# Performance work log

Hardware: AMD Instinct MI355X
Metric: run time of the kernel (lower is better)

## Reference

```python
import jax, jax.numpy as jnp
import numpy as np

EMB = 256
HID = 1024
N_TRACKS = 4096
SEQ = 9
SCALE = 4.0


def setup_inputs() -> dict:
    key = jax.random.key(0)
    ks = jax.random.split(key, 12)

    def init(k, shape, fan_in):
        b = 1.0 / np.sqrt(fan_in)
        return jax.random.uniform(k, shape, jnp.float32, -b, b)

    return {
        "observed": jax.random.normal(ks[0], (SEQ, N_TRACKS, 2), jnp.float32),
        "emb_w": init(ks[1], (EMB - 2, 2), 2),
        "emb_b": init(ks[2], (EMB - 2,), 2),
        "enc_wih": init(ks[3], (4 * HID, EMB), HID),
        "enc_whh": init(ks[4], (4 * HID, HID), HID),
        "enc_b": init(ks[5], (4 * HID,), HID),
        "dec_wih": init(ks[6], (4 * HID, EMB), HID),
        "dec_whh": init(ks[7], (4 * HID, HID), HID),
        "dec_b": init(ks[8], (4 * HID,), HID),
        "h2n_w": init(ks[9], (5, HID), HID),
        "h2n_b": init(ks[10], (5,), HID),
        "n_predict": 12,
    }


def _forward(observed, emb_w, emb_b, enc_wih, enc_whh, enc_b,
             dec_wih, dec_whh, dec_b, h2n_w, h2n_b, n_predict):
    n = observed.shape[1]
    H = enc_whh.shape[1]
    E = enc_wih.shape[1]

    def cell(x, h, c, wih, whh, b):
        # PyTorch LSTMCell gate order: i, f, g, o
        g = x @ wih.T + h @ whh.T + b
        i, f, gg, o = jnp.split(g, 4, axis=-1)
        c = jax.nn.sigmoid(f) * c + jax.nn.sigmoid(i) * jnp.tanh(gg)
        h = jax.nn.sigmoid(o) * jnp.tanh(c)
        return h, c

    def embed(v):
        # Linear(2, E-2) -> ReLU, then 2 zero tag channels
        e = jax.nn.relu((v * SCALE) @ emb_w.T + emb_b)
        return jnp.concatenate([e, jnp.zeros((v.shape[0], 2), e.dtype)], axis=1)

    def h2n(h):
        raw = h @ h2n_w.T + h2n_b
        sig = 0.01 + 0.2 * jax.nn.sigmoid(raw[:, 2:4])  # sigma1, sigma2
        rho = 0.7 * jax.nn.sigmoid(raw[:, 4:5])          # rho
        return jnp.concatenate([raw[:, :2], sig, rho], axis=1)

    def step(params, h, c, obs1, obs2):
        wih, whh, b = params
        mask = ~(jnp.isnan(obs1[:, 0]) | jnp.isnan(obs2[:, 0]))  # [N]
        x = embed(obs2 - obs1)
        h2, c2 = cell(x, h, c, wih, whh, b)
        nrm = h2n(h2)
        m = mask[:, None]
        h = jnp.where(m, h2, h)
        c = jnp.where(m, c2, c)
        normal = jnp.where(m, nrm, jnp.nan)
        pos = obs2 + normal[:, :2]
        return h, c, normal, pos

    h = jnp.zeros((n, H), observed.dtype)
    c = jnp.zeros((n, H), observed.dtype)

    # encoder start tag
    tag_enc = jnp.zeros((n, E), observed.dtype).at[:, -2].set(1.0)
    h, c = cell(tag_enc, h, c, enc_wih, enc_whh, enc_b)

    enc_p = (enc_wih, enc_whh, enc_b)

    def enc_scan(carry, obs_pair):
        h, c = carry
        o1, o2 = obs_pair
        h, c, normal, pos = step(enc_p, h, c, o1, o2)
        return (h, c), (normal, pos)

    (h, c), (enc_normals, enc_positions) = jax.lax.scan(
        enc_scan, (h, c), (observed[:-1], observed[1:]))

    # decoder start tag
    tag_dec = jnp.zeros((n, E), observed.dtype).at[:, -1].set(1.0)
    h, c = cell(tag_dec, h, c, dec_wih, dec_whh, dec_b)

    dec_p = (dec_wih, dec_whh, dec_b)
    p1, p2 = enc_positions[-2], enc_positions[-1]

    def dec_scan(carry, _):
        h, c, p1, p2 = carry
        o1 = jax.lax.stop_gradient(p1)  # .detach() in torch
        o2 = jax.lax.stop_gradient(p2)
        h, c, normal, pos = step(dec_p, h, c, o1, o2)
        return (h, c, p2, pos), (normal, pos)

    _, (dec_normals, dec_positions) = jax.lax.scan(
        dec_scan, (h, c, p1, p2), None, length=n_predict - 1)

    rel_pred_scene = jnp.concatenate([enc_normals, dec_normals], axis=0)
    pred_scene = jnp.concatenate([enc_positions, dec_positions], axis=0)
    return rel_pred_scene, pred_scene


def reference(observed, emb_w, emb_b, enc_wih, enc_whh, enc_b,
              dec_wih, dec_whh, dec_b, h2n_w, h2n_b, n_predict):
    return _forward(observed, emb_w, emb_b, enc_wih, enc_whh, enc_b,
                    dec_wih, dec_whh, dec_b, h2n_w, h2n_b, n_predict)
```

## Files before the change

### kernel.cpp

```cpp
#include <hip/hip_runtime.h>
#include <stdint.h>

#define NTRK 4096
#define HIDN 1024
#define EMBN 256
#define KTOT 1280
#define NOUT 19

typedef __attribute__((ext_vector_type(8))) short short8;
typedef __attribute__((ext_vector_type(4))) float f32x4;

typedef __attribute__((address_space(1))) const void GV;
typedef __attribute__((address_space(3))) void LV;

__device__ __forceinline__ uint16_t f2bf(float f) {
  uint32_t u = __float_as_uint(f);
  u += 0x7fffu + ((u >> 16) & 1u);
  return (uint16_t)(u >> 16);
}
__device__ __forceinline__ float bf2f(uint16_t v) {
  return __uint_as_float(((uint32_t)v) << 16);
}
__device__ __forceinline__ float sigm(float x) { return 1.0f / (1.0f + expf(-x)); }
__device__ __forceinline__ float sigmf_(float x) {
  return __builtin_amdgcn_rcpf(1.0f + __expf(-x));
}
__device__ __forceinline__ float tanhf_(float x) {
  return 2.0f * __builtin_amdgcn_rcpf(1.0f + __expf(-2.0f * x)) - 1.0f;
}

__global__ __launch_bounds__(256) void prep_weights(
    const float* __restrict__ encWih, const float* __restrict__ encWhh,
    const float* __restrict__ encB,
    const float* __restrict__ decWih, const float* __restrict__ decWhh,
    const float* __restrict__ decB,
    uint16_t* __restrict__ WihpE, uint16_t* __restrict__ WhhpE,
    uint16_t* __restrict__ WihpD, uint16_t* __restrict__ WhhpD,
    float* __restrict__ biasE, float* __restrict__ biasD, float* __restrict__ biasDT)
{
  const int jp = blockIdx.x;
  const int q = jp >> 6, r = jp & 63;
  const int gate = r >> 4, l16 = r & 15;
  const int u = q * 16 + l16;
  const int orig = gate * 1024 + u;
  const int t = threadIdx.x;

  WihpE[(size_t)jp * 256 + t] = f2bf(encWih[(size_t)orig * 256 + t]);
  WihpD[(size_t)jp * 256 + t] = f2bf(decWih[(size_t)orig * 256 + t]);
#pragma unroll
  for (int c = 0; c < 4; c++) {
    WhhpE[(size_t)jp * 1024 + c * 256 + t] = f2bf(encWhh[(size_t)orig * 1024 + c * 256 + t]);
    WhhpD[(size_t)jp * 1024 + c * 256 + t] = f2bf(decWhh[(size_t)orig * 1024 + c * 256 + t]);
  }
  if (t == 0) {
    biasE[jp]  = encB[orig];
    biasD[jp]  = decB[orig];
    biasDT[jp] = decB[orig] + decWih[(size_t)orig * 256 + 255];
  }
}

__global__ void init_h0(const float* __restrict__ encWih, const float* __restrict__ encB,
                        float* __restrict__ h0, float* __restrict__ c0)
{
  const int u = blockIdx.x * 256 + threadIdx.x;
  if (u >= 1024) return;
  const float gi = encWih[(size_t)(u) * 256 + 254]        + encB[u];
  const float gg = encWih[(size_t)(2048 + u) * 256 + 254] + encB[2048 + u];
  const float go = encWih[(size_t)(3072 + u) * 256 + 254] + encB[3072 + u];
  const float c = sigm(gi) * tanhf(gg);
  c0[u] = c;
  h0[u] = sigm(go) * tanhf(c);
}

__global__ void fill_state(const float* __restrict__ h0, const float* __restrict__ c0,
                           uint16_t* __restrict__ H, float* __restrict__ Cst)
{
  const size_t i = (size_t)blockIdx.x * 256 + threadIdx.x;
  const int u = (int)(i & 1023);
  H[i] = f2bf(h0[u]);
  Cst[i] = c0[u];
}

__global__ __launch_bounds__(256) void embed_k(
    const float* __restrict__ o1, const float* __restrict__ o2,
    const float* __restrict__ ew, const float* __restrict__ eb,
    uint16_t* __restrict__ X)
{
  const int trk = blockIdx.x;
  const int j = threadIdx.x;
  const float vx = (o2[trk * 2]     - o1[trk * 2])     * 4.0f;
  const float vy = (o2[trk * 2 + 1] - o1[trk * 2 + 1]) * 4.0f;
  float e = 0.f;
  if (j < 254) e = fmaxf(vx * ew[j * 2] + vy * ew[j * 2 + 1] + eb[j], 0.f);
  X[(size_t)trk * 256 + j] = f2bf(e);
}

__global__ __launch_bounds__(256) void embed8(
    const float* __restrict__ observed, const float* __restrict__ ew,
    const float* __restrict__ eb, uint16_t* __restrict__ Xall)
{
  const int t = blockIdx.y;
  const int trk = blockIdx.x;
  const int j = threadIdx.x;
  const float* o1 = observed + ((size_t)t * 4096 + trk) * 2;
  const float* o2 = o1 + 4096 * 2;
  const float vx = (o2[0] - o1[0]) * 4.0f;
  const float vy = (o2[1] - o1[1]) * 4.0f;
  float e = 0.f;
  if (j < 254) e = fmaxf(vx * ew[j * 2] + vy * ew[j * 2 + 1] + eb[j], 0.f);
  Xall[((size_t)t * 4096 + trk) * 256 + j] = f2bf(e);
}

__global__ __launch_bounds__(256) void gemm_lstm(
    const uint16_t* __restrict__ X,   const uint16_t* __restrict__ Hin,
    const uint16_t* __restrict__ Wih, const uint16_t* __restrict__ Whh,
    const float* __restrict__ bias,   float* __restrict__ Cst,
    uint16_t* __restrict__ Hout,
    const float* __restrict__ obs1,   const float* __restrict__ obs2,
    int k0, int maskmode)
{
  __shared__ uint16_t As[128 * 64];
  __shared__ uint16_t Bs[128 * 64];
  __shared__ uint8_t  smask[128];

  const int tid  = threadIdx.x;
  const int wave = tid >> 6;
  const int lane = tid & 63;
  const int bm = blockIdx.y * 128;
  const int bn = blockIdx.x * 128;

  if (tid < 128) {
    bool m = true;
    if (maskmode) {
      const int row = bm + tid;
      const float a = obs1[row * 2];
      const float b = obs2[row * 2];
      m = !((a != a) || (b != b));
    }
    smask[tid] = m ? 1 : 0;
  }

  const int wrow = wave >> 1;
  const int wcol = wave & 1;
  const int quad = lane >> 4;
  const int l15  = lane & 15;
  const int m7   = l15 & 7;
  const int lr = lane >> 3;
  const int lj = ((lane & 7) ^ lr) * 8;

  f32x4 acc[4][4];
#pragma unroll
  for (int i = 0; i < 4; i++)
#pragma unroll
    for (int j = 0; j < 4; j++) acc[i][j] = (f32x4){0.f, 0.f, 0.f, 0.f};

  auto mfma_slab = [&]() {
#pragma unroll
    for (int kk = 0; kk < 64; kk += 32) {
      short8 af[4], bf[4];
      const int jc = (((kk >> 3) + quad) ^ m7) * 8;
#pragma unroll
      for (int i = 0; i < 4; i++) {
        af[i] = *(const short8*)(As + (wrow * 64 + i * 16 + l15) * 64 + jc);
        bf[i] = *(const short8*)(Bs + (wcol * 64 + i * 16 + l15) * 64 + jc);
      }
#pragma unroll
      for (int i = 0; i < 4; i++)
#pragma unroll
        for (int j = 0; j < 4; j++)
          acc[i][j] = __builtin_amdgcn_mfma_f32_16x16x32_bf16(af[i], bf[j], acc[i][j], 0, 0, 0);
    }
  };

  if (k0 == 0) {
    for (int kt = 0; kt < 256; kt += 64) {
      __syncthreads();
#pragma unroll
      for (int cc = 0; cc < 8; cc++) {
        const bool isA = cc < 4;
        const int trow = ((cc & 3) * 4 + wave) * 8;
        const int grow = (isA ? bm : bn) + trow + lr;
        const uint16_t* gsrc = (isA ? X : Wih) + (size_t)grow * 256 + (kt + lj);
        uint16_t* lbase = (isA ? As : Bs) + trow * 64;
        __builtin_amdgcn_global_load_lds((GV*)gsrc, (LV*)lbase, 16, 0, 0);
      }
      __syncthreads();
      mfma_slab();
    }
  }

  for (int kt = 0; kt < 1024; kt += 64) {
    __syncthreads();
#pragma unroll
    for (int cc = 0; cc < 8; cc++) {
      const bool isA = cc < 4;
      const int trow = ((cc & 3) * 4 + wave) * 8;
      const int grow = (isA ? bm : bn) + trow + lr;
      const uint16_t* gsrc = (isA ? Hin : Whh) + (size_t)grow * 1024 + (kt + lj);
      uint16_t* lbase = (isA ? As : Bs) + trow * 64;
      __builtin_amdgcn_global_load_lds((GV*)gsrc, (LV*)lbase, 16, 0, 0);
    }
    __syncthreads();
    mfma_slab();
  }

  const int u  = ((bn >> 6) + wcol) * 16 + l15;
  const int jb = bn + wcol * 64 + l15;
  const float b_i = bias[jb];
  const float b_f = bias[jb + 16];
  const float b_g = bias[jb + 32];
  const float b_o = bias[jb + 48];

#pragma unroll
  for (int mi = 0; mi < 4; mi++) {
#pragma unroll
    for (int r = 0; r < 4; r++) {
      const int row = bm + wrow * 64 + mi * 16 + quad * 4 + r;
      const size_t idx = (size_t)row * 1024 + u;
      uint16_t hv;
      if (smask[row - bm]) {
        const float gi = acc[mi][0][r] + b_i;
        const float gf = acc[mi][1][r] + b_f;
        const float gg = acc[mi][2][r] + b_g;
        const float go = acc[mi][3][r] + b_o;
        const float cn = sigmf_(gf) * Cst[idx] + sigmf_(gi) * tanhf_(gg);
        Cst[idx] = cn;
        hv = f2bf(sigmf_(go) * tanhf_(cn));
      } else {
        hv = Hin[idx];
      }
      Hout[idx] = hv;
    }
  }
}

__global__ __launch_bounds__(256) void h2n_pos(
    const uint16_t* __restrict__ H, const float* __restrict__ w5, const float* __restrict__ b5,
    const float* __restrict__ obs1, const float* __restrict__ obs2,
    float* __restrict__ outrel, float* __restrict__ outpos,
    const float* __restrict__ pprev, const float* __restrict__ ew,
    const float* __restrict__ eb, uint16_t* __restrict__ Xnext, int do_embed)
{
  const int lane  = threadIdx.x & 63;
  const int track = blockIdx.x * 4 + (threadIdx.x >> 6);

  const uint16_t* hrow = H + (size_t)track * 1024 + lane * 16;
  const short8 v0 = *(const short8*)(hrow);
  const short8 v1 = *(const short8*)(hrow + 8);
  float hv[16];
#pragma unroll
  for (int j = 0; j < 8; j++) {
    hv[j]     = bf2f((uint16_t)v0[j]);
    hv[8 + j] = bf2f((uint16_t)v1[j]);
  }
  const int kb = lane * 16;
  float p[5];
#pragma unroll
  for (int o = 0; o < 5; o++) {
    const float* wr = w5 + (size_t)o * 1024 + kb;
    float s = 0.f;
#pragma unroll
    for (int j = 0; j < 16; j++) s += hv[j] * wr[j];
    p[o] = s;
  }
#pragma unroll
  for (int o = 0; o < 5; o++) {
    float v = p[o];
    v += __shfl_xor(v, 32); v += __shfl_xor(v, 16); v += __shfl_xor(v, 8);
    v += __shfl_xor(v, 4);  v += __shfl_xor(v, 2);  v += __shfl_xor(v, 1);
    p[o] = v;
  }
  const float o1x = obs1[track * 2];
  const float o2x = obs2[track * 2];
  const float o2y = obs2[track * 2 + 1];
  const bool msk = !((o1x != o1x) || (o2x != o2x));
  float n0 = p[0] + b5[0];
  float n1 = p[1] + b5[1];
  float n2 = 0.01f + 0.2f * sigmf_(p[2] + b5[2]);
  float n3 = 0.01f + 0.2f * sigmf_(p[3] + b5[3]);
  float n4 = 0.7f  * sigmf_(p[4] + b5[4]);
  if (!msk) {
    const float qn = __uint_as_float(0x7fc00000u);
    n0 = n1 = n2 = n3 = n4 = qn;
  }
  const float posx = o2x + n0;
  const float posy = o2y + n1;
  if (lane == 0) {
    float* rr = outrel + (size_t)track * 5;
    rr[0] = n0; rr[1] = n1; rr[2] = n2; rr[3] = n3; rr[4] = n4;
    outpos[track * 2]     = posx;
    outpos[track * 2 + 1] = posy;
  }
  if (do_embed) {
    const float vx = (posx - pprev[track * 2])     * 4.0f;
    const float vy = (posy - pprev[track * 2 + 1]) * 4.0f;
    uint16_t* xr = Xnext + (size_t)track * 256;
#pragma unroll
    for (int ii = 0; ii < 4; ii++) {
      const int j = ii * 64 + lane;
      float e = 0.f;
      if (j < 254) e = fmaxf(vx * ew[j * 2] + vy * ew[j * 2 + 1] + eb[j], 0.f);
      xr[j] = f2bf(e);
    }
  }
}

extern "C" void kernel_launch(void* const* d_in, const int* in_sizes, int n_in,
                              void* d_out, int out_size, void* d_ws, size_t ws_size,
                              hipStream_t stream)
{
  const float* observed = (const float*)d_in[0];
  const float* emb_w    = (const float*)d_in[1];
  const float* emb_b    = (const float*)d_in[2];
  const float* enc_wih  = (const float*)d_in[3];
  const float* enc_whh  = (const float*)d_in[4];
  const float* enc_b    = (const float*)d_in[5];
  const float* dec_wih  = (const float*)d_in[6];
  const float* dec_whh  = (const float*)d_in[7];
  const float* dec_b    = (const float*)d_in[8];
  const float* h2n_w    = (const float*)d_in[9];
  const float* h2n_b    = (const float*)d_in[10];

  char* ws = (char*)d_ws;
  size_t off = 0;
  auto alloc = [&](size_t bytes) -> void* {
    size_t cur = (off + 255) & ~(size_t)255;
    off = cur + bytes;
    return (void*)(ws + cur);
  };
  uint16_t* WihpE = (uint16_t*)alloc((size_t)4096 * 256 * 2);
  uint16_t* WhhpE = (uint16_t*)alloc((size_t)4096 * 1024 * 2);
  uint16_t* WihpD = (uint16_t*)alloc((size_t)4096 * 256 * 2);
  uint16_t* WhhpD = (uint16_t*)alloc((size_t)4096 * 1024 * 2);
  float*    biasE = (float*)alloc(4096 * 4);
  float*    biasD = (float*)alloc(4096 * 4);
  float*    biasDT= (float*)alloc(4096 * 4);
  float*    h0    = (float*)alloc(1024 * 4);
  float*    c0    = (float*)alloc(1024 * 4);
  uint16_t* HA    = (uint16_t*)alloc((size_t)4096 * 1024 * 2);
  uint16_t* HB    = (uint16_t*)alloc((size_t)4096 * 1024 * 2);
  float*    Cst   = (float*)alloc((size_t)4096 * 1024 * 4);
  uint16_t* Xb    = (uint16_t*)alloc((size_t)4096 * 256 * 2);
  const size_t xall_bytes = (size_t)8 * 4096 * 256 * 2;
  const bool use_xall = (off + 256 + xall_bytes) <= ws_size;
  uint16_t* Xall = use_xall ? (uint16_t*)alloc(xall_bytes) : nullptr;

  float* outrel = (float*)d_out;
  float* outpos = outrel + (size_t)NOUT * 4096 * 5;

  prep_weights<<<4096, 256, 0, stream>>>(enc_wih, enc_whh, enc_b, dec_wih, dec_whh, dec_b,
                                         WihpE, WhhpE, WihpD, WhhpD, biasE, biasD, biasDT);
  init_h0<<<4, 256, 0, stream>>>(enc_wih, enc_b, h0, c0);
  fill_state<<<16384, 256, 0, stream>>>(h0, c0, HA, Cst);
  if (use_xall) {
    embed8<<<dim3(4096, 8), 256, 0, stream>>>(observed, emb_w, emb_b, Xall);
  }

  uint16_t* Hin = HA;
  uint16_t* Hout = HB;
  const dim3 ggrid(32, 32);

  for (int t = 0; t < 8; t++) {
    const float* o1 = observed + (size_t)t * 4096 * 2;
    const float* o2 = observed + (size_t)(t + 1) * 4096 * 2;
    uint16_t* Xt = Xb;
    if (use_xall) {
      Xt = Xall + (size_t)t * 4096 * 256;
    } else {
      embed_k<<<4096, 256, 0, stream>>>(o1, o2, emb_w, emb_b, Xb);
    }
    gemm_lstm<<<ggrid, 256, 0, stream>>>(Xt, Hin, WihpE, WhhpE, biasE, Cst, Hout, o1, o2, 0, 1);
    const int de = (t == 7) ? 1 : 0;
    h2n_pos<<<1024, 256, 0, stream>>>(Hout, h2n_w, h2n_b, o1, o2,
                                      outrel + (size_t)t * 4096 * 5,
                                      outpos + (size_t)t * 4096 * 2,
                                      outpos + (size_t)6 * 4096 * 2, emb_w, emb_b, Xb, de);
    uint16_t* tmp = Hin; Hin = Hout; Hout = tmp;
  }

  gemm_lstm<<<ggrid, 256, 0, stream>>>(nullptr, Hin, WihpD, WhhpD, biasDT, Cst, Hout,
                                       nullptr, nullptr, 256, 0);
  { uint16_t* tmp = Hin; Hin = Hout; Hout = tmp; }

  for (int s = 0; s < 11; s++) {
    const float* p1 = outpos + (size_t)(6 + s) * 4096 * 2;
    const float* p2 = outpos + (size_t)(7 + s) * 4096 * 2;
    gemm_lstm<<<ggrid, 256, 0, stream>>>(Xb, Hin, WihpD, WhhpD, biasD, Cst, Hout, p1, p2, 0, 1);
    const int de = (s < 10) ? 1 : 0;
    h2n_pos<<<1024, 256, 0, stream>>>(Hout, h2n_w, h2n_b, p1, p2,
                                      outrel + (size_t)(8 + s) * 4096 * 5,
                                      outpos + (size_t)(8 + s) * 4096 * 2,
                                      p2, emb_w, emb_b, Xb, de);
    uint16_t* tmp = Hin; Hin = Hout; Hout = tmp;
  }
}
```

Before: 1.460 ms.

## Rewrite LSTM GEMM with 256x256 tiles, 4-stage LDS pipeline and concatenated weights

The input and recurrent weights are packed into one concatenated bf16 matrix of width 1280, so a single K loop covers both parts. The LSTM GEMM kernel moves from 128x128 tiles with 256 threads to 256x256 tiles with 512 threads. It adds a 4-buffer asynchronous global-to-LDS pipeline with three tiles prefetched, plus a remapped block order for better L2 locality. Dummy loads keep the vmcnt bookkeeping uniform at the tail. The goal is to hide load latency and raise operand reuse, at the cost of 128 KB+ of LDS, heavy register pressure from 32 accumulators per lane, and a grid of only 256 blocks.

```diff
diff --git a/kernel.cpp b/kernel.cpp
--- a/kernel.cpp
+++ b/kernel.cpp
@@ -34,8 +34,7 @@
     const float* __restrict__ encB,
     const float* __restrict__ decWih, const float* __restrict__ decWhh,
     const float* __restrict__ decB,
-    uint16_t* __restrict__ WihpE, uint16_t* __restrict__ WhhpE,
-    uint16_t* __restrict__ WihpD, uint16_t* __restrict__ WhhpD,
+    uint16_t* __restrict__ WcatE, uint16_t* __restrict__ WcatD,
     float* __restrict__ biasE, float* __restrict__ biasD, float* __restrict__ biasDT)
 {
   const int jp = blockIdx.x;
@@ -45,12 +44,12 @@
   const int orig = gate * 1024 + u;
   const int t = threadIdx.x;
 
-  WihpE[(size_t)jp * 256 + t] = f2bf(encWih[(size_t)orig * 256 + t]);
-  WihpD[(size_t)jp * 256 + t] = f2bf(decWih[(size_t)orig * 256 + t]);
+  WcatE[(size_t)jp * KTOT + t] = f2bf(encWih[(size_t)orig * 256 + t]);
+  WcatD[(size_t)jp * KTOT + t] = f2bf(decWih[(size_t)orig * 256 + t]);
 #pragma unroll
   for (int c = 0; c < 4; c++) {
-    WhhpE[(size_t)jp * 1024 + c * 256 + t] = f2bf(encWhh[(size_t)orig * 1024 + c * 256 + t]);
-    WhhpD[(size_t)jp * 1024 + c * 256 + t] = f2bf(decWhh[(size_t)orig * 1024 + c * 256 + t]);
+    WcatE[(size_t)jp * KTOT + 256 + c * 256 + t] = f2bf(encWhh[(size_t)orig * 1024 + c * 256 + t]);
+    WcatD[(size_t)jp * KTOT + 256 + c * 256 + t] = f2bf(decWhh[(size_t)orig * 1024 + c * 256 + t]);
   }
   if (t == 0) {
     biasE[jp]  = encB[orig];
@@ -111,111 +110,123 @@
   Xall[((size_t)t * 4096 + trk) * 256 + j] = f2bf(e);
 }
 
-__global__ __launch_bounds__(256) void gemm_lstm(
-    const uint16_t* __restrict__ X,   const uint16_t* __restrict__ Hin,
-    const uint16_t* __restrict__ Wih, const uint16_t* __restrict__ Whh,
-    const float* __restrict__ bias,   float* __restrict__ Cst,
-    uint16_t* __restrict__ Hout,
-    const float* __restrict__ obs1,   const float* __restrict__ obs2,
+__global__ __launch_bounds__(512, 2) void gemm_lstm(
+    const uint16_t* __restrict__ X,    const uint16_t* __restrict__ Hin,
+    const uint16_t* __restrict__ Wcat, const float* __restrict__ bias,
+    float* __restrict__ Cst,           uint16_t* __restrict__ Hout,
+    const float* __restrict__ obs1,    const float* __restrict__ obs2,
     int k0, int maskmode)
 {
-  __shared__ uint16_t As[128 * 64];
-  __shared__ uint16_t Bs[128 * 64];
-  __shared__ uint8_t  smask[128];
+  __shared__ uint16_t As[4 * 8192];
+  __shared__ uint16_t Bs[4 * 8192];
+  __shared__ uint16_t Dm[4096];
+  __shared__ uint8_t  smask[256];
 
   const int tid  = threadIdx.x;
-  const int wave = tid >> 6;
+  const int w    = tid >> 6;
   const int lane = tid & 63;
-  const int bm = blockIdx.y * 128;
-  const int bn = blockIdx.x * 128;
-
-  if (tid < 128) {
+  const int wr   = w >> 2;
+  const int wc   = w & 3;
+  const int quad = lane >> 4;
+  const int l15  = lane & 15;
+
+  const int bid = blockIdx.y * 16 + blockIdx.x;
+  const int wg  = (bid & 7) * 32 + (bid >> 3);
+  const int bm  = (wg >> 4) * 256;
+  const int bn  = (wg & 15) * 256;
+
+  const int NT = (KTOT - k0) >> 5;
+
+  if (tid < 256) {
     bool m = true;
     if (maskmode) {
-      const int row = bm + tid;
-      const float a = obs1[row * 2];
-      const float b = obs2[row * 2];
+      const float a = obs1[(bm + tid) * 2];
+      const float b = obs2[(bm + tid) * 2];
       m = !((a != a) || (b != b));
     }
     smask[tid] = m ? 1 : 0;
   }
 
-  const int wrow = wave >> 1;
-  const int wcol = wave & 1;
-  const int quad = lane >> 4;
-  const int l15  = lane & 15;
-  const int m7   = l15 & 7;
-  const int lr = lane >> 3;
-  const int lj = ((lane & 7) ^ lr) * 8;
-
-  f32x4 acc[4][4];
-#pragma unroll
-  for (int i = 0; i < 4; i++)
+  const int srow = w * 16 + (lane >> 2);
+  const int kch  = (lane & 3) * 8;
+  const uint16_t* pXa = X ? (X + (size_t)(bm + srow) * 256 + kch) : (const uint16_t*)0;
+  const uint16_t* pHa = Hin  + (size_t)(bm + srow) * 1024 + kch;
+  const uint16_t* pBa = Wcat + (size_t)(bn + srow) * (size_t)KTOT + kch;
+  const int ldsw = w * 16 * 32;
+
+  auto stage_tile = [&](int V) {
+    if (V >= NT) {
+      const GV* dsrc = (GV*)(Wcat + (size_t)tid * 8);
+      LV* ddst = (LV*)(Dm + w * 512);
+#pragma unroll
+      for (int uu = 0; uu < 4; uu++)
+        __builtin_amdgcn_global_load_lds(dsrc, ddst, 16, 0, 0);
+      return;
+    }
+    const int kg = k0 + V * 32;
+    uint16_t* asl = As + (V & 3) * 8192;
+    uint16_t* bsl = Bs + (V & 3) * 8192;
+    const uint16_t* a0;
+    int rstride;
+    if (kg < 256) { a0 = pXa + kg;         rstride = 256;  }
+    else          { a0 = pHa + (kg - 256); rstride = 1024; }
+    __builtin_amdgcn_global_load_lds((GV*)a0,                        (LV*)(asl + ldsw),        16, 0, 0);
+    __builtin_amdgcn_global_load_lds((GV*)(a0 + 128 * rstride),      (LV*)(asl + 4096 + ldsw), 16, 0, 0);
+    const uint16_t* b0 = pBa + kg;
+    __builtin_amdgcn_global_load_lds((GV*)b0,                        (LV*)(bsl + ldsw),        16, 0, 0);
+    __builtin_amdgcn_global_load_lds((GV*)(b0 + 128 * KTOT),         (LV*)(bsl + 4096 + ldsw), 16, 0, 0);
+  };
+
+  f32x4 acc[8][4];
+#pragma unroll
+  for (int i = 0; i < 8; i++)
 #pragma unroll
     for (int j = 0; j < 4; j++) acc[i][j] = (f32x4){0.f, 0.f, 0.f, 0.f};
 
-  auto mfma_slab = [&]() {
-#pragma unroll
-    for (int kk = 0; kk < 64; kk += 32) {
-      short8 af[4], bf[4];
-      const int jc = (((kk >> 3) + quad) ^ m7) * 8;
-#pragma unroll
-      for (int i = 0; i < 4; i++) {
-        af[i] = *(const short8*)(As + (wrow * 64 + i * 16 + l15) * 64 + jc);
-        bf[i] = *(const short8*)(Bs + (wcol * 64 + i * 16 + l15) * 64 + jc);
-      }
-#pragma unroll
-      for (int i = 0; i < 4; i++)
-#pragma unroll
-        for (int j = 0; j < 4; j++)
-          acc[i][j] = __builtin_amdgcn_mfma_f32_16x16x32_bf16(af[i], bf[j], acc[i][j], 0, 0, 0);
-    }
-  };
-
-  if (k0 == 0) {
-    for (int kt = 0; kt < 256; kt += 64) {
-      __syncthreads();
-#pragma unroll
-      for (int cc = 0; cc < 8; cc++) {
-        const bool isA = cc < 4;
-        const int trow = ((cc & 3) * 4 + wave) * 8;
-        const int grow = (isA ? bm : bn) + trow + lr;
-        const uint16_t* gsrc = (isA ? X : Wih) + (size_t)grow * 256 + (kt + lj);
-        uint16_t* lbase = (isA ? As : Bs) + trow * 64;
-        __builtin_amdgcn_global_load_lds((GV*)gsrc, (LV*)lbase, 16, 0, 0);
-      }
-      __syncthreads();
-      mfma_slab();
-    }
-  }
-
-  for (int kt = 0; kt < 1024; kt += 64) {
-    __syncthreads();
-#pragma unroll
-    for (int cc = 0; cc < 8; cc++) {
-      const bool isA = cc < 4;
-      const int trow = ((cc & 3) * 4 + wave) * 8;
-      const int grow = (isA ? bm : bn) + trow + lr;
-      const uint16_t* gsrc = (isA ? Hin : Whh) + (size_t)grow * 1024 + (kt + lj);
-      uint16_t* lbase = (isA ? As : Bs) + trow * 64;
-      __builtin_amdgcn_global_load_lds((GV*)gsrc, (LV*)lbase, 16, 0, 0);
-    }
-    __syncthreads();
-    mfma_slab();
-  }
-
-  const int u  = ((bn >> 6) + wcol) * 16 + l15;
-  const int jb = bn + wcol * 64 + l15;
+  stage_tile(0); stage_tile(1); stage_tile(2);
+  asm volatile("s_waitcnt vmcnt(8)" ::: "memory");
+  __builtin_amdgcn_s_barrier();
+
+  const int aoff = (wr * 128 + l15) * 32 + quad * 8;
+  const int boff = (wc * 64  + l15) * 32 + quad * 8;
+
+  for (int T = 0; T < NT; ++T) {
+    stage_tile(T + 3);
+    const uint16_t* asl = As + (T & 3) * 8192;
+    const uint16_t* bsl = Bs + (T & 3) * 8192;
+    short8 bf[4], af[8];
+#pragma unroll
+    for (int n = 0; n < 4; n++)
+      bf[n] = *(const short8*)(bsl + boff + n * 512);
+#pragma unroll
+    for (int m = 0; m < 8; m++)
+      af[m] = *(const short8*)(asl + aoff + m * 512);
+    __builtin_amdgcn_s_setprio(1);
+#pragma unroll
+    for (int m = 0; m < 8; m++)
+#pragma unroll
+      for (int n = 0; n < 4; n++)
+        acc[m][n] = __builtin_amdgcn_mfma_f32_16x16x32_bf16(af[m], bf[n], acc[m][n], 0, 0, 0);
+    __builtin_amdgcn_s_setprio(0);
+    asm volatile("s_waitcnt lgkmcnt(0)" ::: "memory");
+    __builtin_amdgcn_sched_barrier(0);
+    asm volatile("s_waitcnt vmcnt(8)" ::: "memory");
+    __builtin_amdgcn_s_barrier();
+  }
+  asm volatile("s_waitcnt vmcnt(0)" ::: "memory");
+
+  const int u  = ((bn >> 6) + wc) * 16 + l15;
+  const int jb = bn + wc * 64 + l15;
   const float b_i = bias[jb];
   const float b_f = bias[jb + 16];
   const float b_g = bias[jb + 32];
   const float b_o = bias[jb + 48];
 
 #pragma unroll
-  for (int mi = 0; mi < 4; mi++) {
+  for (int mi = 0; mi < 8; mi++) {
 #pragma unroll
     for (int r = 0; r < 4; r++) {
-      const int row = bm + wrow * 64 + mi * 16 + quad * 4 + r;
+      const int row = bm + wr * 128 + mi * 16 + quad * 4 + r;
       const size_t idx = (size_t)row * 1024 + u;
       uint16_t hv;
       if (smask[row - bm]) {
@@ -328,10 +339,8 @@
     off = cur + bytes;
     return (void*)(ws + cur);
   };
-  uint16_t* WihpE = (uint16_t*)alloc((size_t)4096 * 256 * 2);
-  uint16_t* WhhpE = (uint16_t*)alloc((size_t)4096 * 1024 * 2);
-  uint16_t* WihpD = (uint16_t*)alloc((size_t)4096 * 256 * 2);
-  uint16_t* WhhpD = (uint16_t*)alloc((size_t)4096 * 1024 * 2);
+  uint16_t* WcatE = (uint16_t*)alloc((size_t)4096 * KTOT * 2);
+  uint16_t* WcatD = (uint16_t*)alloc((size_t)4096 * KTOT * 2);
   float*    biasE = (float*)alloc(4096 * 4);
   float*    biasD = (float*)alloc(4096 * 4);
   float*    biasDT= (float*)alloc(4096 * 4);
@@ -349,7 +358,7 @@
   float* outpos = outrel + (size_t)NOUT * 4096 * 5;
 
   prep_weights<<<4096, 256, 0, stream>>>(enc_wih, enc_whh, enc_b, dec_wih, dec_whh, dec_b,
-                                         WihpE, WhhpE, WihpD, WhhpD, biasE, biasD, biasDT);
+                                         WcatE, WcatD, biasE, biasD, biasDT);
   init_h0<<<4, 256, 0, stream>>>(enc_wih, enc_b, h0, c0);
   fill_state<<<16384, 256, 0, stream>>>(h0, c0, HA, Cst);
   if (use_xall) {
@@ -358,7 +367,7 @@
 
   uint16_t* Hin = HA;
   uint16_t* Hout = HB;
-  const dim3 ggrid(32, 32);
+  const dim3 ggrid(16, 16);
 
   for (int t = 0; t < 8; t++) {
     const float* o1 = observed + (size_t)t * 4096 * 2;
@@ -369,7 +378,7 @@
     } else {
       embed_k<<<4096, 256, 0, stream>>>(o1, o2, emb_w, emb_b, Xb);
     }
-    gemm_lstm<<<ggrid, 256, 0, stream>>>(Xt, Hin, WihpE, WhhpE, biasE, Cst, Hout, o1, o2, 0, 1);
+    gemm_lstm<<<ggrid, 512, 0, stream>>>(Xt, Hin, WcatE, biasE, Cst, Hout, o1, o2, 0, 1);
     const int de = (t == 7) ? 1 : 0;
     h2n_pos<<<1024, 256, 0, stream>>>(Hout, h2n_w, h2n_b, o1, o2,
                                       outrel + (size_t)t * 4096 * 5,
@@ -378,14 +387,14 @@
     uint16_t* tmp = Hin; Hin = Hout; Hout = tmp;
   }
 
-  gemm_lstm<<<ggrid, 256, 0, stream>>>(nullptr, Hin, WihpD, WhhpD, biasDT, Cst, Hout,
+  gemm_lstm<<<ggrid, 512, 0, stream>>>(nullptr, Hin, WcatD, biasDT, Cst, Hout,
                                        nullptr, nullptr, 256, 0);
   { uint16_t* tmp = Hin; Hin = Hout; Hout = tmp; }
 
   for (int s = 0; s < 11; s++) {
     const float* p1 = outpos + (size_t)(6 + s) * 4096 * 2;
     const float* p2 = outpos + (size_t)(7 + s) * 4096 * 2;
-    gemm_lstm<<<ggrid, 256, 0, stream>>>(Xb, Hin, WihpD, WhhpD, biasD, Cst, Hout, p1, p2, 0, 1);
+    gemm_lstm<<<ggrid, 512, 0, stream>>>(Xb, Hin, WcatD, biasD, Cst, Hout, p1, p2, 0, 1);
     const int de = (s < 10) ? 1 : 0;
     h2n_pos<<<1024, 256, 0, stream>>>(Hout, h2n_w, h2n_b, p1, p2,
                                       outrel + (size_t)(8 + s) * 4096 * 5,
```

Result: faster. 1.309 ms (-10.4%).
